# Performance work log

Measured on AMD Instinct MI355X. Metric: run time of the kernel, lower is better.

The kernel has to match this reference:

```python
import jax, jax.numpy as jnp
import numpy as np
import math

B, L, C, H = 2, 2048, 768, 12
D = C // H
MAX_SCALE_MUL = math.log(100.0)


def setup_inputs() -> dict:
    key = jax.random.key(0)
    ks = jax.random.split(key, 8)
    std = 0.02
    x = jax.random.normal(ks[0], (B, L, C), dtype=jnp.float32)
    attn_bias = jax.random.normal(ks[1], (1, 1, L, L), dtype=jnp.float32)
    W_qkv = jax.random.normal(ks[2], (3 * C, C), dtype=jnp.float32) * std
    b_qkv = jnp.zeros((3 * C,), dtype=jnp.float32)
    # attn_l2_norm=True: learned per-head log-scale, init log(4)
    scale_mul_log = jnp.full((1, H, 1, 1), math.log(4.0), dtype=jnp.float32)
    W_proj = jax.random.normal(ks[3], (C, C), dtype=jnp.float32) * std
    b_proj = jnp.zeros((C,), dtype=jnp.float32)
    return {"x": x, "attn_bias": attn_bias, "W_qkv": W_qkv, "b_qkv": b_qkv,
            "scale_mul_log": scale_mul_log, "W_proj": W_proj, "b_proj": b_proj}


def _l2norm(t):
    # matches F.normalize(dim=-1, eps=1e-12)
    n = jnp.sqrt(jnp.sum(t * t, axis=-1, keepdims=True))
    return t / jnp.maximum(n, 1e-12)


def reference(x, attn_bias, W_qkv, b_qkv, scale_mul_log, W_proj, b_proj):
    Bx, Lx, Cx = x.shape
    qkv = (x @ W_qkv.T + b_qkv).reshape(Bx, Lx, 3, H, D)
    # -> [3, B, H, L, D]
    qkv = jnp.transpose(qkv, (2, 0, 3, 1, 4))
    q, k, v = qkv[0], qkv[1], qkv[2]
    scale_mul = jnp.exp(jnp.minimum(scale_mul_log, MAX_SCALE_MUL))  # [1,H,1,1]
    q = _l2norm(q) * scale_mul
    k = _l2norm(k)
    # scale = 1 in the l2-norm branch
    attn = jnp.einsum('bhqd,bhkd->bhqk', q, k) + attn_bias
    attn = jax.nn.softmax(attn, axis=-1)
    oup = jnp.einsum('bhqk,bhkd->bhqd', attn, v)          # [B,H,L,D]
    oup = jnp.transpose(oup, (0, 2, 1, 3)).reshape(Bx, Lx, Cx)
    return oup @ W_proj.T + b_proj
```

## Files before the change

kernel.cpp:

```cpp
#include <hip/hip_runtime.h>
#include <math.h>

#define B_ 2
#define L_ 2048
#define C_ 768
#define H_ 12
#define D_ 64
#define M_ (B_ * L_)
#define MAXLOG 4.605170185988091f

typedef __bf16 bf16;
typedef __bf16 bf16x4 __attribute__((ext_vector_type(4)));
typedef __bf16 bf16x8 __attribute__((ext_vector_type(8)));
typedef float  f32x4  __attribute__((ext_vector_type(4)));

#define SZ_  ((size_t)B_ * H_ * L_ * D_)
#define MC_  ((size_t)M_ * C_)
#define WQ_  ((size_t)3 * C_ * C_)
#define WP_  ((size_t)C_ * C_)

__global__ __launch_bounds__(256) void prep(
    const float4* __restrict__ x, const float4* __restrict__ Wq,
    const float4* __restrict__ Wp,
    bf16* __restrict__ xb, bf16* __restrict__ wqb,
    bf16* __restrict__ Wh, bf16* __restrict__ Wl,
    float4* __restrict__ zbase)
{
    const int X4 = (int)(MC_ / 4);
    const int W4 = (int)(WQ_ / 4);
    const int S4 = (int)(WP_ / 4);
    const int Z4 = (int)((3 * SZ_ + 2 * MC_) * sizeof(bf16) / 16);
    const int total = X4 + W4 + S4 + Z4;

    const int i0 = blockIdx.x * 256 + threadIdx.x;
    const int stride = gridDim.x * 256;
    for (int i = i0; i < total; i += stride) {
        if (i < X4) {
            const float4 v = x[i];
            bf16x4 o; o[0]=(bf16)v.x; o[1]=(bf16)v.y; o[2]=(bf16)v.z; o[3]=(bf16)v.w;
            *(bf16x4*)&xb[(size_t)i * 4] = o;
        } else if (i < X4 + W4) {
            const int j = i - X4;
            const float4 v = Wq[j];
            bf16x4 o; o[0]=(bf16)v.x; o[1]=(bf16)v.y; o[2]=(bf16)v.z; o[3]=(bf16)v.w;
            *(bf16x4*)&wqb[(size_t)j * 4] = o;
        } else if (i < X4 + W4 + S4) {
            const int j = i - X4 - W4;
            const float4 v = Wp[j];
            bf16x4 h, l;
            h[0]=(bf16)v.x; l[0]=(bf16)(v.x-(float)h[0]);
            h[1]=(bf16)v.y; l[1]=(bf16)(v.y-(float)h[1]);
            h[2]=(bf16)v.z; l[2]=(bf16)(v.z-(float)h[2]);
            h[3]=(bf16)v.w; l[3]=(bf16)(v.w-(float)h[3]);
            *(bf16x4*)&Wh[(size_t)j * 4] = h;
            *(bf16x4*)&Wl[(size_t)j * 4] = l;
        } else {
            zbase[i - X4 - W4 - S4] = (float4){0.f, 0.f, 0.f, 0.f};
        }
    }
}

__global__ __launch_bounds__(256) void qkv_mfma(
    const bf16* __restrict__ A, const bf16* __restrict__ W,
    const float* __restrict__ bias, const float* __restrict__ sml,
    bf16* __restrict__ qb, bf16* __restrict__ kb, bf16* __restrict__ vtb)
{
    __shared__ __align__(16) bf16 As[128][72];
    __shared__ __align__(16) bf16 Bs[64][72];

    const int t    = threadIdx.x;
    const int w    = t >> 6;
    const int lane = t & 63;
    const int quad = lane >> 4;
    const int c    = lane & 15;
    const int m0   = blockIdx.x * 128;
    const int n0   = blockIdx.y * 64;

    f32x4 acc[2][4];
    #pragma unroll
    for (int mt = 0; mt < 2; ++mt)
        #pragma unroll
        for (int nt = 0; nt < 4; ++nt) acc[mt][nt] = (f32x4){0.f,0.f,0.f,0.f};

    for (int kt = 0; kt < C_; kt += 64) {
        __syncthreads();
        #pragma unroll
        for (int p = 0; p < 4; ++p) {
            const int idx = t + p * 256;
            const int row = idx >> 3;
            const int cg  = (idx & 7) * 8;
            *(bf16x8*)&As[row][cg] = *(const bf16x8*)&A[(size_t)(m0 + row) * C_ + kt + cg];
        }
        #pragma unroll
        for (int p = 0; p < 2; ++p) {
            const int idx = t + p * 256;
            const int row = idx >> 3;
            const int cg  = (idx & 7) * 8;
            *(bf16x8*)&Bs[row][cg] = *(const bf16x8*)&W[(size_t)(n0 + row) * C_ + kt + cg];
        }
        __syncthreads();

        #pragma unroll
        for (int ks = 0; ks < 2; ++ks) {
            #pragma unroll
            for (int mt = 0; mt < 2; ++mt) {
                const bf16x8 a = *(const bf16x8*)&As[w * 32 + mt * 16 + c][ks * 32 + quad * 8];
                #pragma unroll
                for (int nt = 0; nt < 4; ++nt) {
                    const bf16x8 b = *(const bf16x8*)&Bs[nt * 16 + c][ks * 32 + quad * 8];
                    acc[mt][nt] = __builtin_amdgcn_mfma_f32_16x16x32_bf16(a, b, acc[mt][nt], 0, 0, 0);
                }
            }
        }
    }

    const int three = blockIdx.y / H_;
    const int h     = blockIdx.y % H_;
    const int bidx  = m0 >> 11;
    const int l0    = (m0 & (L_ - 1)) + w * 32;

    if (three < 2) {
        bf16* dst = (three == 0) ? qb : kb;
        const float scale = (three == 0) ? expf(fminf(sml[h], MAXLOG)) : 1.0f;
        #pragma unroll
        for (int mt = 0; mt < 2; ++mt) {
            float val[4][4];
            float ss[4] = {0.f, 0.f, 0.f, 0.f};
            #pragma unroll
            for (int nt = 0; nt < 4; ++nt) {
                const float bb = bias[n0 + nt * 16 + c];
                #pragma unroll
                for (int reg = 0; reg < 4; ++reg) {
                    const float v = acc[mt][nt][reg] + bb;
                    val[nt][reg] = v;
                    ss[reg] += v * v;
                }
            }
            #pragma unroll
            for (int reg = 0; reg < 4; ++reg) {
                float s = ss[reg];
                #pragma unroll
                for (int off = 1; off < 16; off <<= 1) s += __shfl_xor(s, off, 16);
                const float inv = scale / fmaxf(sqrtf(s), 1e-12f);
                const int l = l0 + mt * 16 + quad * 4 + reg;
                #pragma unroll
                for (int nt = 0; nt < 4; ++nt)
                    dst[((size_t)(bidx * H_ + h) * L_ + l) * D_ + nt * 16 + c] =
                        (bf16)(val[nt][reg] * inv);
            }
        }
    } else {
        #pragma unroll
        for (int mt = 0; mt < 2; ++mt)
            #pragma unroll
            for (int nt = 0; nt < 4; ++nt) {
                const int d = nt * 16 + c;
                const float bb = bias[n0 + d];
                const int l = l0 + mt * 16 + quad * 4;
                bf16x4 o;
                #pragma unroll
                for (int reg = 0; reg < 4; ++reg) o[reg] = (bf16)(acc[mt][nt][reg] + bb);
                *(bf16x4*)&vtb[((size_t)(bidx * H_ + h) * D_ + d) * L_ + l] = o;
            }
    }
}

__global__ __launch_bounds__(256) void flash_mfma(
    const bf16* __restrict__ q, const bf16* __restrict__ k,
    const bf16* __restrict__ vt, const float* __restrict__ bias,
    const float* __restrict__ sml,
    bf16* __restrict__ aoh, bf16* __restrict__ aol)
{
    __shared__ __align__(16) bf16 Qs [64][72];
    __shared__ __align__(16) bf16 Ks [64][72];
    __shared__ __align__(16) bf16 Vts[64][72];
    __shared__ __align__(16) bf16 Ps [64][72];

    const int t    = threadIdx.x;
    const int w    = t >> 6;
    const int lane = t & 63;
    const int quad = lane >> 4;
    const int c    = lane & 15;
    const int q0   = blockIdx.x * 64;
    const int bh   = blockIdx.y;
    const int h    = bh % H_;
    const int b    = bh / H_;
    const size_t base  = (size_t)bh * L_ * D_;
    const size_t vbase = (size_t)bh * D_ * L_;

    const float scale = expf(fminf(sml[h], MAXLOG));
    const float FMAX  = scale + 8.0f;

    #pragma unroll
    for (int p = 0; p < 2; ++p) {
        const int f = t + p * 256;
        const int r = f >> 3, d0 = (f & 7) * 8;
        *(bf16x8*)&Qs[r][d0] = *(const bf16x8*)&q[base + (size_t)(q0 + r) * D_ + d0];
    }
    __syncthreads();

    float l_acc[4] = {0.f, 0.f, 0.f, 0.f};
    f32x4 O[4];
    #pragma unroll
    for (int i = 0; i < 4; ++i) O[i] = (f32x4){0.f, 0.f, 0.f, 0.f};

    const int rbase = q0 + w * 16 + quad * 4;

    for (int kt = 0; kt < L_; kt += 64) {
        __syncthreads();
        #pragma unroll
        for (int p = 0; p < 2; ++p) {
            const int f = t + p * 256;
            const int r = f >> 3, c0 = (f & 7) * 8;
            *(bf16x8*)&Ks [r][c0] = *(const bf16x8*)&k [base  + (size_t)(kt + r) * D_ + c0];
            *(bf16x8*)&Vts[r][c0] = *(const bf16x8*)&vt[vbase + (size_t)r * L_ + kt + c0];
        }

        f32x4 S[4];
        #pragma unroll
        for (int tile = 0; tile < 4; ++tile)
            #pragma unroll
            for (int reg = 0; reg < 4; ++reg)
                S[tile][reg] = bias[(size_t)(rbase + reg) * L_ + kt + tile * 16 + c];
        __syncthreads();

        #pragma unroll
        for (int ks = 0; ks < 2; ++ks) {
            const bf16x8 a = *(const bf16x8*)&Qs[w * 16 + c][ks * 32 + quad * 8];
            #pragma unroll
            for (int tile = 0; tile < 4; ++tile) {
                const bf16x8 bb = *(const bf16x8*)&Ks[tile * 16 + c][ks * 32 + quad * 8];
                S[tile] = __builtin_amdgcn_mfma_f32_16x16x32_bf16(a, bb, S[tile], 0, 0, 0);
            }
        }

        #pragma unroll
        for (int tile = 0; tile < 4; ++tile)
            #pragma unroll
            for (int reg = 0; reg < 4; ++reg) {
                const float pv = __expf(S[tile][reg] - FMAX);
                l_acc[reg] += pv;
                Ps[w * 16 + quad * 4 + reg][tile * 16 + c] = (bf16)pv;
            }
        __syncthreads();

        #pragma unroll
        for (int ks = 0; ks < 2; ++ks) {
            const bf16x8 a = *(const bf16x8*)&Ps[w * 16 + c][ks * 32 + quad * 8];
            #pragma unroll
            for (int tile = 0; tile < 4; ++tile) {
                const bf16x8 bb = *(const bf16x8*)&Vts[tile * 16 + c][ks * 32 + quad * 8];
                O[tile] = __builtin_amdgcn_mfma_f32_16x16x32_bf16(a, bb, O[tile], 0, 0, 0);
            }
        }
    }

    #pragma unroll
    for (int reg = 0; reg < 4; ++reg) {
        float rs = l_acc[reg];
        #pragma unroll
        for (int off = 1; off < 16; off <<= 1) rs += __shfl_xor(rs, off, 16);
        const float linv = 1.0f / rs;
        const int   row  = q0 + w * 16 + quad * 4 + reg;
        const size_t o   = ((size_t)(b * L_ + row)) * C_ + h * 64 + c;
        #pragma unroll
        for (int tile = 0; tile < 4; ++tile) {
            const float v  = O[tile][reg] * linv;
            const bf16  hv = (bf16)v;
            aoh[o + tile * 16] = hv;
            aol[o + tile * 16] = (bf16)(v - (float)hv);
        }
    }
}

__global__ __launch_bounds__(256) void proj_mfma(
    const bf16* __restrict__ Ahg, const bf16* __restrict__ Alg,
    const bf16* __restrict__ Whg, const bf16* __restrict__ Wlg,
    const float* __restrict__ bias, float* __restrict__ outp)
{
    __shared__ __align__(16) bf16 Ah[128][72];
    __shared__ __align__(16) bf16 Al[128][72];
    __shared__ __align__(16) bf16 Bh[64][72];
    __shared__ __align__(16) bf16 Bl[64][72];

    const int t    = threadIdx.x;
    const int w    = t >> 6;
    const int lane = t & 63;
    const int quad = lane >> 4;
    const int c    = lane & 15;
    const int m0   = blockIdx.x * 128;
    const int n0   = blockIdx.y * 64;

    f32x4 acc[2][4];
    #pragma unroll
    for (int mt = 0; mt < 2; ++mt)
        #pragma unroll
        for (int nt = 0; nt < 4; ++nt) acc[mt][nt] = (f32x4){0.f,0.f,0.f,0.f};

    for (int kt = 0; kt < C_; kt += 64) {
        __syncthreads();
        #pragma unroll
        for (int p = 0; p < 4; ++p) {
            const int idx = t + p * 256;
            const int row = idx >> 3;
            const int cg  = (idx & 7) * 8;
            *(bf16x8*)&Ah[row][cg] = *(const bf16x8*)&Ahg[(size_t)(m0 + row) * C_ + kt + cg];
            *(bf16x8*)&Al[row][cg] = *(const bf16x8*)&Alg[(size_t)(m0 + row) * C_ + kt + cg];
        }
        #pragma unroll
        for (int p = 0; p < 2; ++p) {
            const int idx = t + p * 256;
            const int row = idx >> 3;
            const int cg  = (idx & 7) * 8;
            *(bf16x8*)&Bh[row][cg] = *(const bf16x8*)&Whg[(size_t)(n0 + row) * C_ + kt + cg];
            *(bf16x8*)&Bl[row][cg] = *(const bf16x8*)&Wlg[(size_t)(n0 + row) * C_ + kt + cg];
        }
        __syncthreads();

        #pragma unroll
        for (int ks = 0; ks < 2; ++ks) {
            #pragma unroll
            for (int mt = 0; mt < 2; ++mt) {
                const bf16x8 ah = *(const bf16x8*)&Ah[w * 32 + mt * 16 + c][ks * 32 + quad * 8];
                const bf16x8 al = *(const bf16x8*)&Al[w * 32 + mt * 16 + c][ks * 32 + quad * 8];
                #pragma unroll
                for (int nt = 0; nt < 4; ++nt) {
                    const bf16x8 bh = *(const bf16x8*)&Bh[nt * 16 + c][ks * 32 + quad * 8];
                    const bf16x8 bl = *(const bf16x8*)&Bl[nt * 16 + c][ks * 32 + quad * 8];
                    acc[mt][nt] = __builtin_amdgcn_mfma_f32_16x16x32_bf16(ah, bh, acc[mt][nt], 0, 0, 0);
                    acc[mt][nt] = __builtin_amdgcn_mfma_f32_16x16x32_bf16(ah, bl, acc[mt][nt], 0, 0, 0);
                    acc[mt][nt] = __builtin_amdgcn_mfma_f32_16x16x32_bf16(al, bh, acc[mt][nt], 0, 0, 0);
                }
            }
        }
    }

    #pragma unroll
    for (int mt = 0; mt < 2; ++mt)
        #pragma unroll
        for (int nt = 0; nt < 4; ++nt) {
            const int col = n0 + nt * 16 + c;
            const float bb = bias[col];
            #pragma unroll
            for (int reg = 0; reg < 4; ++reg) {
                const int row = m0 + w * 32 + mt * 16 + quad * 4 + reg;
                outp[(size_t)row * C_ + col] = acc[mt][nt][reg] + bb;
            }
        }
}

extern "C" void kernel_launch(void* const* d_in, const int* in_sizes, int n_in,
                              void* d_out, int out_size, void* d_ws, size_t ws_size,
                              hipStream_t stream)
{
    const float* x         = (const float*)d_in[0];
    const float* attn_bias = (const float*)d_in[1];
    const float* W_qkv     = (const float*)d_in[2];
    const float* b_qkv     = (const float*)d_in[3];
    const float* sml       = (const float*)d_in[4];
    const float* W_proj    = (const float*)d_in[5];
    const float* b_proj    = (const float*)d_in[6];
    float* out = (float*)d_out;

    bf16* qb  = (bf16*)d_ws;
    bf16* kb  = qb  + SZ_;
    bf16* vtb = kb  + SZ_;
    bf16* aoh = vtb + SZ_;
    bf16* aol = aoh + MC_;
    bf16* Wh  = aol + MC_;
    bf16* Wl  = Wh  + WP_;
    bf16* xb  = Wl  + WP_;
    bf16* wqb = xb  + MC_;

    prep<<<2048, 256, 0, stream>>>(
        (const float4*)x, (const float4*)W_qkv, (const float4*)W_proj,
        xb, wqb, Wh, Wl, (float4*)qb);

    qkv_mfma<<<dim3(M_ / 128, (3 * C_) / 64), 256, 0, stream>>>(
        xb, wqb, b_qkv, sml, qb, kb, vtb);

    flash_mfma<<<dim3(L_ / 64, B_ * H_), 256, 0, stream>>>(
        qb, kb, vtb, attn_bias, sml, aoh, aol);

    proj_mfma<<<dim3(M_ / 128, C_ / 64), 256, 0, stream>>>(
        aoh, aol, Wh, Wl, b_proj, out);
}
```

Before: 214.1 us.

## Split flash attention over key halves and fuse combine into projection

```diff
diff --git a/kernel.cpp b/kernel.cpp
--- a/kernel.cpp
+++ b/kernel.cpp
@@ -18,19 +18,22 @@
 #define MC_  ((size_t)M_ * C_)
 #define WQ_  ((size_t)3 * C_ * C_)
 #define WP_  ((size_t)C_ * C_)
+#define BHL_ ((size_t)B_ * H_ * L_)
 
 __global__ __launch_bounds__(256) void prep(
     const float4* __restrict__ x, const float4* __restrict__ Wq,
     const float4* __restrict__ Wp,
     bf16* __restrict__ xb, bf16* __restrict__ wqb,
     bf16* __restrict__ Wh, bf16* __restrict__ Wl,
-    float4* __restrict__ zbase)
+    float4* __restrict__ zA, float4* __restrict__ zB)
 {
-    const int X4 = (int)(MC_ / 4);
-    const int W4 = (int)(WQ_ / 4);
-    const int S4 = (int)(WP_ / 4);
-    const int Z4 = (int)((3 * SZ_ + 2 * MC_) * sizeof(bf16) / 16);
-    const int total = X4 + W4 + S4 + Z4;
+    const int X4  = (int)(MC_ / 4);
+    const int W4  = (int)(WQ_ / 4);
+    const int S4  = (int)(WP_ / 4);
+    const int Z4a = (int)(3 * SZ_ * sizeof(bf16) / 16);
+    const int Z4b = (int)((2 * SZ_ * sizeof(float) + 2 * BHL_ * sizeof(float)
+                           - (MC_ + WQ_) * sizeof(bf16)) / 16);
+    const int total = X4 + W4 + S4 + Z4a + Z4b;
 
     const int i0 = blockIdx.x * 256 + threadIdx.x;
     const int stride = gridDim.x * 256;
@@ -54,8 +57,10 @@
             h[3]=(bf16)v.w; l[3]=(bf16)(v.w-(float)h[3]);
             *(bf16x4*)&Wh[(size_t)j * 4] = h;
             *(bf16x4*)&Wl[(size_t)j * 4] = l;
+        } else if (i < X4 + W4 + S4 + Z4a) {
+            zA[i - X4 - W4 - S4] = (float4){0.f, 0.f, 0.f, 0.f};
         } else {
-            zbase[i - X4 - W4 - S4] = (float4){0.f, 0.f, 0.f, 0.f};
+            zB[i - X4 - W4 - S4 - Z4a] = (float4){0.f, 0.f, 0.f, 0.f};
         }
     }
 }
@@ -165,48 +170,54 @@
     }
 }
 
-__global__ __launch_bounds__(256) void flash_mfma(
+__global__ __launch_bounds__(256, 4) void flash_mfma(
     const bf16* __restrict__ q, const bf16* __restrict__ k,
     const bf16* __restrict__ vt, const float* __restrict__ bias,
     const float* __restrict__ sml,
-    bf16* __restrict__ aoh, bf16* __restrict__ aol)
+    float* __restrict__ Opart, float* __restrict__ lpart)
 {
-    __shared__ __align__(16) bf16 Qs [64][72];
+    __shared__ __align__(16) bf16 QPs[128][72];
     __shared__ __align__(16) bf16 Ks [64][72];
     __shared__ __align__(16) bf16 Vts[64][72];
-    __shared__ __align__(16) bf16 Ps [64][72];
-
-    const int t    = threadIdx.x;
-    const int w    = t >> 6;
-    const int lane = t & 63;
-    const int quad = lane >> 4;
-    const int c    = lane & 15;
-    const int q0   = blockIdx.x * 64;
-    const int bh   = blockIdx.y;
-    const int h    = bh % H_;
-    const int b    = bh / H_;
+
+    const int t     = threadIdx.x;
+    const int w     = t >> 6;
+    const int lane  = t & 63;
+    const int quad  = lane >> 4;
+    const int c     = lane & 15;
+    const int q0    = blockIdx.x * 128;
+    const int bh    = blockIdx.y;
+    const int split = blockIdx.z;
+    const int kt0   = split * (L_ / 2);
     const size_t base  = (size_t)bh * L_ * D_;
     const size_t vbase = (size_t)bh * D_ * L_;
 
-    const float scale = expf(fminf(sml[h], MAXLOG));
-    const float FMAX  = scale + 8.0f;
-
-    #pragma unroll
-    for (int p = 0; p < 2; ++p) {
+    const float FMAX = expf(fminf(sml[bh % H_], MAXLOG)) + 8.0f;
+
+    #pragma unroll
+    for (int p = 0; p < 4; ++p) {
         const int f = t + p * 256;
         const int r = f >> 3, d0 = (f & 7) * 8;
-        *(bf16x8*)&Qs[r][d0] = *(const bf16x8*)&q[base + (size_t)(q0 + r) * D_ + d0];
+        *(bf16x8*)&QPs[r][d0] = *(const bf16x8*)&q[base + (size_t)(q0 + r) * D_ + d0];
     }
     __syncthreads();
-
-    float l_acc[4] = {0.f, 0.f, 0.f, 0.f};
-    f32x4 O[4];
-    #pragma unroll
-    for (int i = 0; i < 4; ++i) O[i] = (f32x4){0.f, 0.f, 0.f, 0.f};
-
-    const int rbase = q0 + w * 16 + quad * 4;
-
-    for (int kt = 0; kt < L_; kt += 64) {
+    bf16x8 Qreg[2][2];
+    #pragma unroll
+    for (int mt = 0; mt < 2; ++mt)
+        #pragma unroll
+        for (int ks = 0; ks < 2; ++ks)
+            Qreg[mt][ks] = *(const bf16x8*)&QPs[w * 32 + mt * 16 + c][ks * 32 + quad * 8];
+    __syncthreads();
+
+    float l_acc[2][4] = {};
+    f32x4 O[2][4];
+    #pragma unroll
+    for (int mt = 0; mt < 2; ++mt)
+        #pragma unroll
+        for (int nt = 0; nt < 4; ++nt) O[mt][nt] = (f32x4){0.f, 0.f, 0.f, 0.f};
+
+    for (int it = 0; it < L_ / 2; it += 64) {
+        const int kt = kt0 + it;
         __syncthreads();
         #pragma unroll
         for (int p = 0; p < 2; ++p) {
@@ -216,65 +227,82 @@
             *(bf16x8*)&Vts[r][c0] = *(const bf16x8*)&vt[vbase + (size_t)r * L_ + kt + c0];
         }
 
-        f32x4 S[4];
-        #pragma unroll
-        for (int tile = 0; tile < 4; ++tile)
-            #pragma unroll
-            for (int reg = 0; reg < 4; ++reg)
-                S[tile][reg] = bias[(size_t)(rbase + reg) * L_ + kt + tile * 16 + c];
+        f32x4 S[2][4];
+        #pragma unroll
+        for (int mt = 0; mt < 2; ++mt) {
+            const int rb = q0 + w * 32 + mt * 16 + quad * 4;
+            #pragma unroll
+            for (int nt = 0; nt < 4; ++nt)
+                #pragma unroll
+                for (int reg = 0; reg < 4; ++reg)
+                    S[mt][nt][reg] = bias[(size_t)(rb + reg) * L_ + kt + nt * 16 + c];
+        }
         __syncthreads();
 
         #pragma unroll
         for (int ks = 0; ks < 2; ++ks) {
-            const bf16x8 a = *(const bf16x8*)&Qs[w * 16 + c][ks * 32 + quad * 8];
-            #pragma unroll
-            for (int tile = 0; tile < 4; ++tile) {
-                const bf16x8 bb = *(const bf16x8*)&Ks[tile * 16 + c][ks * 32 + quad * 8];
-                S[tile] = __builtin_amdgcn_mfma_f32_16x16x32_bf16(a, bb, S[tile], 0, 0, 0);
-            }
-        }
-
-        #pragma unroll
-        for (int tile = 0; tile < 4; ++tile)
-            #pragma unroll
-            for (int reg = 0; reg < 4; ++reg) {
-                const float pv = __expf(S[tile][reg] - FMAX);
-                l_acc[reg] += pv;
-                Ps[w * 16 + quad * 4 + reg][tile * 16 + c] = (bf16)pv;
-            }
+            bf16x8 bb[4];
+            #pragma unroll
+            for (int nt = 0; nt < 4; ++nt)
+                bb[nt] = *(const bf16x8*)&Ks[nt * 16 + c][ks * 32 + quad * 8];
+            #pragma unroll
+            for (int mt = 0; mt < 2; ++mt)
+                #pragma unroll
+                for (int nt = 0; nt < 4; ++nt)
+                    S[mt][nt] = __builtin_amdgcn_mfma_f32_16x16x32_bf16(
+                        Qreg[mt][ks], bb[nt], S[mt][nt], 0, 0, 0);
+        }
+
+        #pragma unroll
+        for (int mt = 0; mt < 2; ++mt)
+            #pragma unroll
+            for (int nt = 0; nt < 4; ++nt)
+                #pragma unroll
+                for (int reg = 0; reg < 4; ++reg) {
+                    const float pv = __expf(S[mt][nt][reg] - FMAX);
+                    l_acc[mt][reg] += pv;
+                    QPs[w * 32 + mt * 16 + quad * 4 + reg][nt * 16 + c] = (bf16)pv;
+                }
         __syncthreads();
 
         #pragma unroll
         for (int ks = 0; ks < 2; ++ks) {
-            const bf16x8 a = *(const bf16x8*)&Ps[w * 16 + c][ks * 32 + quad * 8];
-            #pragma unroll
-            for (int tile = 0; tile < 4; ++tile) {
-                const bf16x8 bb = *(const bf16x8*)&Vts[tile * 16 + c][ks * 32 + quad * 8];
-                O[tile] = __builtin_amdgcn_mfma_f32_16x16x32_bf16(a, bb, O[tile], 0, 0, 0);
-            }
-        }
-    }
-
-    #pragma unroll
-    for (int reg = 0; reg < 4; ++reg) {
-        float rs = l_acc[reg];
-        #pragma unroll
-        for (int off = 1; off < 16; off <<= 1) rs += __shfl_xor(rs, off, 16);
-        const float linv = 1.0f / rs;
-        const int   row  = q0 + w * 16 + quad * 4 + reg;
-        const size_t o   = ((size_t)(b * L_ + row)) * C_ + h * 64 + c;
-        #pragma unroll
-        for (int tile = 0; tile < 4; ++tile) {
-            const float v  = O[tile][reg] * linv;
-            const bf16  hv = (bf16)v;
-            aoh[o + tile * 16] = hv;
-            aol[o + tile * 16] = (bf16)(v - (float)hv);
-        }
-    }
+            bf16x8 bb[4];
+            #pragma unroll
+            for (int nt = 0; nt < 4; ++nt)
+                bb[nt] = *(const bf16x8*)&Vts[nt * 16 + c][ks * 32 + quad * 8];
+            #pragma unroll
+            for (int mt = 0; mt < 2; ++mt) {
+                const bf16x8 a = *(const bf16x8*)&QPs[w * 32 + mt * 16 + c][ks * 32 + quad * 8];
+                #pragma unroll
+                for (int nt = 0; nt < 4; ++nt)
+                    O[mt][nt] = __builtin_amdgcn_mfma_f32_16x16x32_bf16(
+                        a, bb[nt], O[mt][nt], 0, 0, 0);
+            }
+        }
+    }
+
+    float* lp = lpart + (size_t)split * BHL_ + (size_t)bh * L_;
+    float* op = Opart + (size_t)split * SZ_;
+    #pragma unroll
+    for (int mt = 0; mt < 2; ++mt)
+        #pragma unroll
+        for (int reg = 0; reg < 4; ++reg) {
+            float rs = l_acc[mt][reg];
+            #pragma unroll
+            for (int off = 1; off < 16; off <<= 1) rs += __shfl_xor(rs, off, 16);
+            const int row = q0 + w * 32 + mt * 16 + quad * 4 + reg;
+            if (c == 0) lp[row] = rs;
+            const size_t ob = ((size_t)bh * L_ + row) * D_;
+            #pragma unroll
+            for (int nt = 0; nt < 4; ++nt)
+                op[ob + nt * 16 + c] = O[mt][nt][reg];
+        }
 }
 
 __global__ __launch_bounds__(256) void proj_mfma(
-    const bf16* __restrict__ Ahg, const bf16* __restrict__ Alg,
+    const float* __restrict__ Op0, const float* __restrict__ Op1,
+    const float* __restrict__ lp0, const float* __restrict__ lp1,
     const bf16* __restrict__ Whg, const bf16* __restrict__ Wlg,
     const float* __restrict__ bias, float* __restrict__ outp)
 {
@@ -298,14 +326,37 @@
         for (int nt = 0; nt < 4; ++nt) acc[mt][nt] = (f32x4){0.f,0.f,0.f,0.f};
 
     for (int kt = 0; kt < C_; kt += 64) {
+        const int h = kt >> 6;
         __syncthreads();
         #pragma unroll
         for (int p = 0; p < 4; ++p) {
             const int idx = t + p * 256;
-            const int row = idx >> 3;
+            const int rl  = idx >> 3;
             const int cg  = (idx & 7) * 8;
-            *(bf16x8*)&Ah[row][cg] = *(const bf16x8*)&Ahg[(size_t)(m0 + row) * C_ + kt + cg];
-            *(bf16x8*)&Al[row][cg] = *(const bf16x8*)&Alg[(size_t)(m0 + row) * C_ + kt + cg];
+            const int row = m0 + rl;
+            const int bi  = row >> 11;
+            const int l   = row & (L_ - 1);
+            const size_t bhrow = ((size_t)(bi * H_ + h) * L_ + l);
+            const float linv = 1.0f / (lp0[bhrow] + lp1[bhrow]);
+            const float* a0 = &Op0[bhrow * D_ + cg];
+            const float* a1 = &Op1[bhrow * D_ + cg];
+            const float4 u0 = *(const float4*)a0;
+            const float4 u1 = *(const float4*)(a0 + 4);
+            const float4 v0 = *(const float4*)a1;
+            const float4 v1 = *(const float4*)(a1 + 4);
+            float vals[8];
+            vals[0] = (u0.x + v0.x) * linv; vals[1] = (u0.y + v0.y) * linv;
+            vals[2] = (u0.z + v0.z) * linv; vals[3] = (u0.w + v0.w) * linv;
+            vals[4] = (u1.x + v1.x) * linv; vals[5] = (u1.y + v1.y) * linv;
+            vals[6] = (u1.z + v1.z) * linv; vals[7] = (u1.w + v1.w) * linv;
+            bf16x8 hv, lv;
+            #pragma unroll
+            for (int j = 0; j < 8; ++j) {
+                hv[j] = (bf16)vals[j];
+                lv[j] = (bf16)(vals[j] - (float)hv[j]);
+            }
+            *(bf16x8*)&Ah[rl][cg] = hv;
+            *(bf16x8*)&Al[rl][cg] = lv;
         }
         #pragma unroll
         for (int p = 0; p < 2; ++p) {
@@ -365,23 +416,27 @@
     bf16* qb  = (bf16*)d_ws;
     bf16* kb  = qb  + SZ_;
     bf16* vtb = kb  + SZ_;
-    bf16* aoh = vtb + SZ_;
-    bf16* aol = aoh + MC_;
-    bf16* Wh  = aol + MC_;
+    bf16* Wh  = vtb + SZ_;
     bf16* Wl  = Wh  + WP_;
     bf16* xb  = Wl  + WP_;
     bf16* wqb = xb  + MC_;
+    float* Op0 = (float*)xb;
+    float* Op1 = Op0 + SZ_;
+    float* lp0 = Op0 + 2 * SZ_;
+    float* lp1 = lp0 + BHL_;
+    float4* zA = (float4*)qb;
+    float4* zB = (float4*)(wqb + WQ_);
 
     prep<<<2048, 256, 0, stream>>>(
         (const float4*)x, (const float4*)W_qkv, (const float4*)W_proj,
-        xb, wqb, Wh, Wl, (float4*)qb);
+        xb, wqb, Wh, Wl, zA, zB);
 
     qkv_mfma<<<dim3(M_ / 128, (3 * C_) / 64), 256, 0, stream>>>(
         xb, wqb, b_qkv, sml, qb, kb, vtb);
 
-    flash_mfma<<<dim3(L_ / 64, B_ * H_), 256, 0, stream>>>(
-        qb, kb, vtb, attn_bias, sml, aoh, aol);
+    flash_mfma<<<dim3(L_ / 128, B_ * H_, 2), 256, 0, stream>>>(
+        qb, kb, vtb, attn_bias, sml, Op0, lp0);
 
     proj_mfma<<<dim3(M_ / 128, C_ / 64), 256, 0, stream>>>(
-        aoh, aol, Wh, Wl, b_proj, out);
+        Op0, Op1, lp0, lp1, Wh, Wl, b_proj, out);
 }
```

Measured after the change: 229.1 us. 1.07x slower.

## Prefetch next K/V/bias tile into registers and keep Q in registers

Applied to the files above, without the earlier changes.

```diff
diff --git a/kernel.cpp b/kernel.cpp
--- a/kernel.cpp
+++ b/kernel.cpp
@@ -171,10 +171,9 @@
     const float* __restrict__ sml,
     bf16* __restrict__ aoh, bf16* __restrict__ aol)
 {
-    __shared__ __align__(16) bf16 Qs [64][72];
+    __shared__ __align__(16) bf16 QPs[64][72];
     __shared__ __align__(16) bf16 Ks [64][72];
     __shared__ __align__(16) bf16 Vts[64][72];
-    __shared__ __align__(16) bf16 Ps [64][72];
 
     const int t    = threadIdx.x;
     const int w    = t >> 6;
@@ -188,49 +187,76 @@
     const size_t base  = (size_t)bh * L_ * D_;
     const size_t vbase = (size_t)bh * D_ * L_;
 
-    const float scale = expf(fminf(sml[h], MAXLOG));
-    const float FMAX  = scale + 8.0f;
+    const float FMAX = expf(fminf(sml[h], MAXLOG)) + 8.0f;
 
     #pragma unroll
     for (int p = 0; p < 2; ++p) {
         const int f = t + p * 256;
         const int r = f >> 3, d0 = (f & 7) * 8;
-        *(bf16x8*)&Qs[r][d0] = *(const bf16x8*)&q[base + (size_t)(q0 + r) * D_ + d0];
+        *(bf16x8*)&QPs[r][d0] = *(const bf16x8*)&q[base + (size_t)(q0 + r) * D_ + d0];
     }
     __syncthreads();
+    bf16x8 Qreg[2];
+    Qreg[0] = *(const bf16x8*)&QPs[w * 16 + c][quad * 8];
+    Qreg[1] = *(const bf16x8*)&QPs[w * 16 + c][32 + quad * 8];
+
+    const int rbase = q0 + w * 16 + quad * 4;
+
+    const int r0  = t >> 3,        c00 = (t & 7) * 8;
+    const int r1  = (t + 256) >> 3, c01 = ((t + 256) & 7) * 8;
+
+    bf16x8 kreg[2], vreg[2];
+    float  breg[4][4];
+    kreg[0] = *(const bf16x8*)&k [base  + (size_t)r0 * D_ + c00];
+    kreg[1] = *(const bf16x8*)&k [base  + (size_t)r1 * D_ + c01];
+    vreg[0] = *(const bf16x8*)&vt[vbase + (size_t)r0 * L_ + c00];
+    vreg[1] = *(const bf16x8*)&vt[vbase + (size_t)r1 * L_ + c01];
+    #pragma unroll
+    for (int tile = 0; tile < 4; ++tile)
+        #pragma unroll
+        for (int reg = 0; reg < 4; ++reg)
+            breg[tile][reg] = bias[(size_t)(rbase + reg) * L_ + tile * 16 + c];
 
     float l_acc[4] = {0.f, 0.f, 0.f, 0.f};
     f32x4 O[4];
     #pragma unroll
     for (int i = 0; i < 4; ++i) O[i] = (f32x4){0.f, 0.f, 0.f, 0.f};
 
-    const int rbase = q0 + w * 16 + quad * 4;
-
     for (int kt = 0; kt < L_; kt += 64) {
         __syncthreads();
-        #pragma unroll
-        for (int p = 0; p < 2; ++p) {
-            const int f = t + p * 256;
-            const int r = f >> 3, c0 = (f & 7) * 8;
-            *(bf16x8*)&Ks [r][c0] = *(const bf16x8*)&k [base  + (size_t)(kt + r) * D_ + c0];
-            *(bf16x8*)&Vts[r][c0] = *(const bf16x8*)&vt[vbase + (size_t)r * L_ + kt + c0];
-        }
+
+        *(bf16x8*)&Ks [r0][c00] = kreg[0];
+        *(bf16x8*)&Ks [r1][c01] = kreg[1];
+        *(bf16x8*)&Vts[r0][c00] = vreg[0];
+        *(bf16x8*)&Vts[r1][c01] = vreg[1];
 
         f32x4 S[4];
         #pragma unroll
         for (int tile = 0; tile < 4; ++tile)
             #pragma unroll
             for (int reg = 0; reg < 4; ++reg)
-                S[tile][reg] = bias[(size_t)(rbase + reg) * L_ + kt + tile * 16 + c];
+                S[tile][reg] = breg[tile][reg];
+
+        const int kt2 = kt + 64;
+        if (kt2 < L_) {
+            kreg[0] = *(const bf16x8*)&k [base  + (size_t)(kt2 + r0) * D_ + c00];
+            kreg[1] = *(const bf16x8*)&k [base  + (size_t)(kt2 + r1) * D_ + c01];
+            vreg[0] = *(const bf16x8*)&vt[vbase + (size_t)r0 * L_ + kt2 + c00];
+            vreg[1] = *(const bf16x8*)&vt[vbase + (size_t)r1 * L_ + kt2 + c01];
+            #pragma unroll
+            for (int tile = 0; tile < 4; ++tile)
+                #pragma unroll
+                for (int reg = 0; reg < 4; ++reg)
+                    breg[tile][reg] = bias[(size_t)(rbase + reg) * L_ + kt2 + tile * 16 + c];
+        }
         __syncthreads();
 
         #pragma unroll
         for (int ks = 0; ks < 2; ++ks) {
-            const bf16x8 a = *(const bf16x8*)&Qs[w * 16 + c][ks * 32 + quad * 8];
             #pragma unroll
             for (int tile = 0; tile < 4; ++tile) {
                 const bf16x8 bb = *(const bf16x8*)&Ks[tile * 16 + c][ks * 32 + quad * 8];
-                S[tile] = __builtin_amdgcn_mfma_f32_16x16x32_bf16(a, bb, S[tile], 0, 0, 0);
+                S[tile] = __builtin_amdgcn_mfma_f32_16x16x32_bf16(Qreg[ks], bb, S[tile], 0, 0, 0);
             }
         }
 
@@ -240,13 +266,13 @@
             for (int reg = 0; reg < 4; ++reg) {
                 const float pv = __expf(S[tile][reg] - FMAX);
                 l_acc[reg] += pv;
-                Ps[w * 16 + quad * 4 + reg][tile * 16 + c] = (bf16)pv;
+                QPs[w * 16 + quad * 4 + reg][tile * 16 + c] = (bf16)pv;
             }
         __syncthreads();
 
         #pragma unroll
         for (int ks = 0; ks < 2; ++ks) {
-            const bf16x8 a = *(const bf16x8*)&Ps[w * 16 + c][ks * 32 + quad * 8];
+            const bf16x8 a = *(const bf16x8*)&QPs[w * 16 + c][ks * 32 + quad * 8];
             #pragma unroll
             for (int tile = 0; tile < 4; ++tile) {
                 const bf16x8 bb = *(const bf16x8*)&Vts[tile * 16 + c][ks * 32 + quad * 8];
```

New measurement: 209.4 us. 1.02x faster.
